# Performance work log

Measured on AMD Instinct MI355X. Metric: run time of the kernel, lower is better.

Reference implementation:

```python
import jax, jax.numpy as jnp
import numpy as np

# dissected_Conv2d forward: grouped conv (groups=in_channels) producing one
# feature map per (input_channel, output_channel) pair, then permute_add_featuremaps:
# a gather by add_perm followed by a segmented sum over input channels, plus bias.

IN_C, OUT_C = 64, 64
KH, KW = 3, 3
B, H, W = 8, 56, 56
PAD = 1


def setup_inputs() -> dict:
    key = jax.random.key(0)
    k1, k2, k3 = jax.random.split(key, 3)
    x = jax.random.normal(k1, (B, IN_C, H, W), dtype=jnp.float32)
    # from_conv.weight: [out_channels, in_channels, kh, kw]
    weight = jax.random.normal(k2, (OUT_C, IN_C, KH, KW), dtype=jnp.float32) * 0.05
    bias = jax.random.normal(k3, (OUT_C,), dtype=jnp.float32) * 0.05
    return {"x": x, "weight": weight, "bias": bias}


def reference(x, weight, bias):
    out_c, in_c, kh, kw = weight.shape
    # make_preadd_conv: weight.view(in*out, 1, kh, kw)[weight_perm].
    # weight_perm maps grouped-conv channel k = i*out + j  ->  W[j, i], i.e. a
    # (out,in) -> (in,out) transpose of the leading dims.
    w_grp = jnp.transpose(weight, (1, 0, 2, 3)).reshape(in_c * out_c, 1, kh, kw)
    # grouped conv, groups = in_channels: group i convolves input channel i with
    # out_c kernels, giving preadd[:, i*out + j] = conv2d(x[:, i], W[j, i]).
    preadd = jax.lax.conv_general_dilated(
        x, w_grp,
        window_strides=(1, 1),
        padding=((PAD, PAD), (PAD, PAD)),
        dimension_numbers=("NCHW", "OIHW", "NCHW"),
        feature_group_count=in_c,
    )  # [B, in*out, H, W]
    # permute_add_featuremaps: gather with add_perm (channel p = o*in + i pulls
    # preadd channel i*out + o), then split/cat/sum == reshape [B,out,in,H,W].sum(in).
    p = jnp.arange(out_c * in_c)
    add_perm = (p % in_c) * out_c + p // in_c
    gathered = preadd[:, add_perm]  # [B, out*in, H, W]
    b_, _, h_, w_ = gathered.shape
    summed = gathered.reshape(b_, out_c, in_c, h_, w_).sum(axis=2)  # [B, out, H, W]
    # bias add: from_conv.bias.unsqueeze(1).unsqueeze(1) broadcast over H, W
    return summed + bias[None, :, None, None]
```

## Files before the change

kernel.cpp:

```cpp
#include <hip/hip_runtime.h>


typedef __attribute__((ext_vector_type(8))) short bf8_t;
typedef __attribute__((ext_vector_type(4))) float f4_t;

#define IC 64
#define OC 64
#define HH 56
#define WW 56
#define NB 8
#define ROWS 2
#define RB (HH / ROWS)
#define NPIX (ROWS * WW)
#define NT (NPIX / 16)
#define LC (WW + 2)
#define LR (ROWS + 2)
#define NS ((IC * 9) / 32)
#define WSTRIDE 578

__device__ __forceinline__ unsigned short f2bf(float f) {
    unsigned u = __float_as_uint(f);
    return (unsigned short)((u + 0x7FFFu + ((u >> 16) & 1u)) >> 16);
}

__global__ __launch_bounds__(256)
void conv3x3_mfma(const float* __restrict__ x, const float* __restrict__ w,
                  const float* __restrict__ bias, float* __restrict__ out) {
    __shared__ unsigned short lds[OC * WSTRIDE];

    const int tid  = threadIdx.x;
    const int wv   = tid >> 6;
    const int lane = tid & 63;
    const int kg   = lane >> 4;
    const int l15  = lane & 15;

    const int bx = blockIdx.x;
    const int b  = bx / RB;
    const int h0 = (bx - b * RB) * ROWS;

    for (int i4 = tid; i4 < (OC * IC * 9) / 4; i4 += 256) {
        const float4 v = ((const float4*)w)[i4];
        const int e0  = i4 * 4;
        const int oc  = e0 / 576;
        const int rem = e0 - oc * 576;
        unsigned* dst = (unsigned*)&lds[oc * WSTRIDE + rem];
        dst[0] = (unsigned)f2bf(v.x) | ((unsigned)f2bf(v.y) << 16);
        dst[1] = (unsigned)f2bf(v.z) | ((unsigned)f2bf(v.w) << 16);
    }
    __syncthreads();

    const int oc_a = wv * 16 + l15;
    bf8_t afrag[NS];
    #pragma unroll
    for (int s = 0; s < NS; ++s) {
        const int tap = s >> 1;
        const int ic0 = (s & 1) * 32 + kg * 8;
        #pragma unroll
        for (int j = 0; j < 8; ++j) {
            afrag[s][j] = (short)lds[oc_a * WSTRIDE + (ic0 + j) * 9 + tap];
        }
    }
    __syncthreads();

    {
        const int col  = lane;
        const int wcol = col - 1;
        const bool cok = (col < LC);
        const bool wok = (wcol >= 0) && (wcol < WW);
        #pragma unroll
        for (int q = 0; q < 8; ++q) {
            const int combo = wv * 8 + q;
            const int icb = combo >> 2;
            const int r   = combo & 3;
            const int h   = h0 - 1 + r;
            const bool ok = cok && wok && (h >= 0) && (h < HH);
            bf8_t v;
            #pragma unroll
            for (int j = 0; j < 8; ++j) {
                float f = 0.f;
                if (ok) f = x[(((b * IC) + icb * 8 + j) * HH + h) * WW + wcol];
                v[j] = (short)f2bf(f);
            }
            if (cok) *(bf8_t*)&lds[((icb * LR + r) * LC + col) * 8] = v;
        }
    }
    __syncthreads();

    f4_t acc[NT];
    #pragma unroll
    for (int t = 0; t < NT; ++t) acc[t] = 0.f;

    int pixoff[NT], prow[NT], pcol[NT];
    #pragma unroll
    for (int t = 0; t < NT; ++t) {
        const int p  = t * 16 + l15;
        const int rp = p / WW;
        const int cp = p - rp * WW;
        prow[t] = rp;
        pcol[t] = cp;
        pixoff[t] = (rp * LC + cp) * 16;
    }
    const char* base = (const char*)lds + kg * (LR * LC * 16);

    #pragma unroll
    for (int s = 0; s < NS; ++s) {
        const int tap  = s >> 1;
        const int khh  = tap / 3;
        const int kww  = tap - khh * 3;
        const int soff = (s & 1) * (4 * LR * LC * 16) + (khh * LC + kww) * 16;
        #pragma unroll
        for (int t = 0; t < NT; ++t) {
            bf8_t bv = *(const bf8_t*)(base + soff + pixoff[t]);
            acc[t] = __builtin_amdgcn_mfma_f32_16x16x32_bf16(afrag[s], bv, acc[t], 0, 0, 0);
        }
    }

    const int oc_c = wv * 16 + kg * 4;
    const float b0 = bias[oc_c + 0];
    const float b1 = bias[oc_c + 1];
    const float b2 = bias[oc_c + 2];
    const float b3 = bias[oc_c + 3];
    #pragma unroll
    for (int t = 0; t < NT; ++t) {
        const int h = h0 + prow[t];
        const int cp = pcol[t];
        float* o = &out[((b * OC + oc_c) * HH + h) * WW + cp];
        o[0 * HH * WW] = acc[t][0] + b0;
        o[1 * HH * WW] = acc[t][1] + b1;
        o[2 * HH * WW] = acc[t][2] + b2;
        o[3 * HH * WW] = acc[t][3] + b3;
    }
}

extern "C" void kernel_launch(void* const* d_in, const int* in_sizes, int n_in,
                              void* d_out, int out_size, void* d_ws, size_t ws_size,
                              hipStream_t stream) {
    const float* x    = (const float*)d_in[0];
    const float* w    = (const float*)d_in[1];
    const float* bias = (const float*)d_in[2];
    float* out        = (float*)d_out;
    hipLaunchKernelGGL(conv3x3_mfma, dim3(NB * RB), dim3(256), 0, stream,
                       x, w, bias, out);
}
```

Measured before the change: 82.99 us.

## Split conv into input NHWC-bf16 prep, weight repack, and LDS-free main kernel

Replaces the single fused kernel with three launches. The first converts x to a zero-padded NHWC bf16 buffer in workspace, the second repacks the weights into MFMA fragment order, and the main kernel reads both directly from global memory without LDS, each block handling 32 pixels. The aim is to stop every block from redundantly converting all 64x576 weights and staging input into LDS, and to get many more, smaller blocks for occupancy. In exchange it adds two extra kernel launches and a round trip of the converted input through global memory, and the main loop relies on cache hits for the overlapping 3x3 reads.

Measured after the change: 89.46 us. 1.08x slower.

```diff
diff --git a/kernel.cpp b/kernel.cpp
--- a/kernel.cpp
+++ b/kernel.cpp
@@ -9,14 +9,14 @@
 #define HH 56
 #define WW 56
 #define NB 8
-#define ROWS 2
-#define RB (HH / ROWS)
-#define NPIX (ROWS * WW)
-#define NT (NPIX / 16)
-#define LC (WW + 2)
-#define LR (ROWS + 2)
-#define NS ((IC * 9) / 32)
-#define WSTRIDE 578
+#define PH 58
+#define PW 58
+#define NS 18
+#define NPIX (HH * WW)
+#define PT 98
+
+#define XT_BYTES (NB * PH * PW * IC * 2)
+#define LPAD 68
 
 __device__ __forceinline__ unsigned short f2bf(float f) {
     unsigned u = __float_as_uint(f);
@@ -24,111 +24,110 @@
 }
 
 __global__ __launch_bounds__(256)
-void conv3x3_mfma(const float* __restrict__ x, const float* __restrict__ w,
-                  const float* __restrict__ bias, float* __restrict__ out) {
-    __shared__ unsigned short lds[OC * WSTRIDE];
+void prep_x(const float* __restrict__ x, unsigned short* __restrict__ xt) {
+    const int bx  = blockIdx.x;
+    const int tid = threadIdx.x;
+    if (bx < NB * HH) {
+        const int b = bx / HH, h = bx - (bx / HH) * HH;
+        __shared__ unsigned short lds[WW * LPAD];
+        for (int idx = tid; idx < IC * WW; idx += 256) {
+            const int ic = idx / WW, w = idx - (idx / WW) * WW;
+            lds[w * LPAD + ic] = f2bf(x[((b * IC + ic) * HH + h) * WW + w]);
+        }
+        __syncthreads();
+        for (int idx = tid; idx < WW * 16; idx += 256) {
+            const int w = idx >> 4, icq = idx & 15;
+            const uint2 v = *(const uint2*)&lds[w * LPAD + icq * 4];
+            *(uint2*)&xt[((b * PH + h + 1) * PW + (w + 1)) * IC + icq * 4] = v;
+        }
+    } else {
+        const int b = bx - NB * HH;
+        unsigned short* base = xt + (size_t)b * PH * PW * IC;
+        for (int i = tid; i < 1824; i += 256) {
+            int off;
+            if (i < 464)        off = i * 8;
+            else if (i < 928)   off = 57 * PW * IC + (i - 464) * 8;
+            else if (i < 1376) { int j = i - 928;  off = (1 + (j >> 3)) * PW * IC + (j & 7) * 8; }
+            else               { int j = i - 1376; off = (1 + (j >> 3)) * PW * IC + 57 * IC + (j & 7) * 8; }
+            *(uint4*)(base + off) = uint4{0, 0, 0, 0};
+        }
+    }
+}
 
+__global__ __launch_bounds__(256)
+void repack_w(const float* __restrict__ w, unsigned short* __restrict__ wf) {
+    const int s    = blockIdx.x;
+    const int tid  = threadIdx.x;
+    const int wv   = tid >> 6;
+    const int lane = tid & 63;
+    const int oc   = wv * 16 + (lane & 15);
+    const int kg   = lane >> 4;
+    const int tap  = s >> 1;
+    const int ic0  = (s & 1) * 32 + kg * 8;
+    unsigned short tmp[8];
+    #pragma unroll
+    for (int j = 0; j < 8; ++j)
+        tmp[j] = f2bf(w[(oc * IC + ic0 + j) * 9 + tap]);
+    *(uint4*)&wf[(((s * 4 + wv) * 64) + lane) * 8] = *(const uint4*)tmp;
+}
+
+__global__ __launch_bounds__(256)
+void conv_main(const unsigned short* __restrict__ xt,
+               const unsigned short* __restrict__ wf,
+               const float* __restrict__ bias,
+               float* __restrict__ out) {
+    const int bx   = blockIdx.x;
+    const int b    = bx / PT;
+    const int pt   = bx - b * PT;
+    const int p0   = pt * 32;
     const int tid  = threadIdx.x;
     const int wv   = tid >> 6;
     const int lane = tid & 63;
     const int kg   = lane >> 4;
     const int l15  = lane & 15;
 
-    const int bx = blockIdx.x;
-    const int b  = bx / RB;
-    const int h0 = (bx - b * RB) * ROWS;
-
-    for (int i4 = tid; i4 < (OC * IC * 9) / 4; i4 += 256) {
-        const float4 v = ((const float4*)w)[i4];
-        const int e0  = i4 * 4;
-        const int oc  = e0 / 576;
-        const int rem = e0 - oc * 576;
-        unsigned* dst = (unsigned*)&lds[oc * WSTRIDE + rem];
-        dst[0] = (unsigned)f2bf(v.x) | ((unsigned)f2bf(v.y) << 16);
-        dst[1] = (unsigned)f2bf(v.z) | ((unsigned)f2bf(v.w) << 16);
-    }
-    __syncthreads();
-
-    const int oc_a = wv * 16 + l15;
     bf8_t afrag[NS];
     #pragma unroll
-    for (int s = 0; s < NS; ++s) {
-        const int tap = s >> 1;
-        const int ic0 = (s & 1) * 32 + kg * 8;
-        #pragma unroll
-        for (int j = 0; j < 8; ++j) {
-            afrag[s][j] = (short)lds[oc_a * WSTRIDE + (ic0 + j) * 9 + tap];
-        }
+    for (int s = 0; s < NS; ++s)
+        afrag[s] = *(const bf8_t*)&wf[(((s * 4 + wv) * 64) + lane) * 8];
+
+    const char* pbase0;
+    const char* pbase1;
+    int pp0, pp1;
+    {
+        const int p = p0 + l15;
+        const int hp = p / WW, wp = p - (p / WW) * WW;
+        pp0 = p;
+        pbase0 = (const char*)xt +
+                 ((size_t)b * PH * PW * IC + ((hp * PW + wp) * IC) + kg * 8) * 2;
     }
-    __syncthreads();
+    {
+        const int p = p0 + 16 + l15;
+        const int hp = p / WW, wp = p - (p / WW) * WW;
+        pp1 = p;
+        pbase1 = (const char*)xt +
+                 ((size_t)b * PH * PW * IC + ((hp * PW + wp) * IC) + kg * 8) * 2;
+    }
 
-    {
-        const int col  = lane;
-        const int wcol = col - 1;
-        const bool cok = (col < LC);
-        const bool wok = (wcol >= 0) && (wcol < WW);
-        #pragma unroll
-        for (int q = 0; q < 8; ++q) {
-            const int combo = wv * 8 + q;
-            const int icb = combo >> 2;
-            const int r   = combo & 3;
-            const int h   = h0 - 1 + r;
-            const bool ok = cok && wok && (h >= 0) && (h < HH);
-            bf8_t v;
-            #pragma unroll
-            for (int j = 0; j < 8; ++j) {
-                float f = 0.f;
-                if (ok) f = x[(((b * IC) + icb * 8 + j) * HH + h) * WW + wcol];
-                v[j] = (short)f2bf(f);
-            }
-            if (cok) *(bf8_t*)&lds[((icb * LR + r) * LC + col) * 8] = v;
-        }
-    }
-    __syncthreads();
-
-    f4_t acc[NT];
-    #pragma unroll
-    for (int t = 0; t < NT; ++t) acc[t] = 0.f;
-
-    int pixoff[NT], prow[NT], pcol[NT];
-    #pragma unroll
-    for (int t = 0; t < NT; ++t) {
-        const int p  = t * 16 + l15;
-        const int rp = p / WW;
-        const int cp = p - rp * WW;
-        prow[t] = rp;
-        pcol[t] = cp;
-        pixoff[t] = (rp * LC + cp) * 16;
-    }
-    const char* base = (const char*)lds + kg * (LR * LC * 16);
+    f4_t acc0 = {0.f, 0.f, 0.f, 0.f};
+    f4_t acc1 = {0.f, 0.f, 0.f, 0.f};
 
     #pragma unroll
     for (int s = 0; s < NS; ++s) {
         const int tap  = s >> 1;
-        const int khh  = tap / 3;
-        const int kww  = tap - khh * 3;
-        const int soff = (s & 1) * (4 * LR * LC * 16) + (khh * LC + kww) * 16;
-        #pragma unroll
-        for (int t = 0; t < NT; ++t) {
-            bf8_t bv = *(const bf8_t*)(base + soff + pixoff[t]);
-            acc[t] = __builtin_amdgcn_mfma_f32_16x16x32_bf16(afrag[s], bv, acc[t], 0, 0, 0);
-        }
+        const int soff = ((tap / 3) * PW + (tap % 3)) * IC * 2 + (s & 1) * 64;
+        const bf8_t bv0 = *(const bf8_t*)(pbase0 + soff);
+        const bf8_t bv1 = *(const bf8_t*)(pbase1 + soff);
+        acc0 = __builtin_amdgcn_mfma_f32_16x16x32_bf16(afrag[s], bv0, acc0, 0, 0, 0);
+        acc1 = __builtin_amdgcn_mfma_f32_16x16x32_bf16(afrag[s], bv1, acc1, 0, 0, 0);
     }
 
     const int oc_c = wv * 16 + kg * 4;
-    const float b0 = bias[oc_c + 0];
-    const float b1 = bias[oc_c + 1];
-    const float b2 = bias[oc_c + 2];
-    const float b3 = bias[oc_c + 3];
     #pragma unroll
-    for (int t = 0; t < NT; ++t) {
-        const int h = h0 + prow[t];
-        const int cp = pcol[t];
-        float* o = &out[((b * OC + oc_c) * HH + h) * WW + cp];
-        o[0 * HH * WW] = acc[t][0] + b0;
-        o[1 * HH * WW] = acc[t][1] + b1;
-        o[2 * HH * WW] = acc[t][2] + b2;
-        o[3 * HH * WW] = acc[t][3] + b3;
+    for (int rr = 0; rr < 4; ++rr) {
+        const float bb = bias[oc_c + rr];
+        out[(b * OC + oc_c + rr) * NPIX + pp0] = acc0[rr] + bb;
+        out[(b * OC + oc_c + rr) * NPIX + pp1] = acc1[rr] + bb;
     }
 }
 
@@ -139,6 +138,12 @@
     const float* w    = (const float*)d_in[1];
     const float* bias = (const float*)d_in[2];
     float* out        = (float*)d_out;
-    hipLaunchKernelGGL(conv3x3_mfma, dim3(NB * RB), dim3(256), 0, stream,
-                       x, w, bias, out);
+
+    unsigned short* xt = (unsigned short*)d_ws;
+    unsigned short* wf = (unsigned short*)((char*)d_ws + XT_BYTES);
+
+    hipLaunchKernelGGL(prep_x,   dim3(NB * HH + NB), dim3(256), 0, stream, x, xt);
+    hipLaunchKernelGGL(repack_w, dim3(NS),           dim3(256), 0, stream, w, wf);
+    hipLaunchKernelGGL(conv_main, dim3(NB * PT),     dim3(256), 0, stream,
+                       xt, wf, bias, out);
 }
```
